# Performance work log

Measured on AMD Instinct MI355X. Metric: run time of the kernel, lower is better.

Reference implementation:

```python
import jax, jax.numpy as jnp
import numpy as np

N_NODES = 8192
D = 384
N_EDGES = 262144
N_REL = 4
N_LAYERS = 2
BATCH = 64


def setup_inputs() -> dict:
    key = jax.random.key(0)
    ks = jax.random.split(key, 8)
    x = jax.random.normal(ks[0], (N_NODES, D), jnp.float32)
    edge_index = jax.random.randint(ks[1], (2, N_EDGES), 0, N_NODES, dtype=jnp.int32)
    edge_type = jax.random.randint(ks[2], (N_EDGES,), 0, N_REL, dtype=jnp.int32)
    s = 1.0 / np.sqrt(D)
    W_rel = jax.random.uniform(ks[3], (N_LAYERS, N_REL, D, D), jnp.float32, -s, s)
    b_rel = jnp.zeros((N_LAYERS, N_REL, D), jnp.float32)
    norm_const = jnp.ones((N_LAYERS, N_REL), jnp.float32)
    W_msg = jax.random.uniform(ks[4], (N_LAYERS, D, D), jnp.float32, -s, s)
    b_msg = jnp.zeros((N_LAYERS, D), jnp.float32)
    W_self = jax.random.uniform(ks[5], (N_LAYERS, D, D), jnp.float32, -s, s)
    b_self = jnp.zeros((N_LAYERS, D), jnp.float32)
    bn_gamma = jnp.ones((D,), jnp.float32)
    bn_beta = jnp.zeros((D,), jnp.float32)
    return {"x": x, "edge_index": edge_index, "edge_type": edge_type,
            "bn_gamma": bn_gamma, "bn_beta": bn_beta,
            "W_rel": W_rel, "b_rel": b_rel, "norm_const": norm_const,
            "W_msg": W_msg, "b_msg": b_msg, "W_self": W_self, "b_self": b_self,
            "batch_size": BATCH}


def _seg_sum(v, idx, n):
    return jax.ops.segment_sum(v, idx, num_segments=n)


def _forward(x, bn_gamma, bn_beta, W_rel, b_rel, norm_const, W_msg, b_msg,
             W_self, b_self, edge_index, edge_type, batch_size):
    n = x.shape[0]
    # BatchNorm1d (training-mode batch stats) on the utterance embeddings
    mu = x.mean(axis=0)
    var = x.var(axis=0)
    h = bn_gamma * (x - mu) * jax.lax.rsqrt(var + 1e-5) + bn_beta
    src, dst = edge_index[0], edge_index[1]  # PyG: row=source(j), col=target(i)
    # pairwise cosine similarity, gathered only at the edges actually used:
    # edge_weights[dst, src] = <h_dst, h_src> / (|h_dst||h_src|)
    xn = h / jnp.linalg.norm(h, axis=1, keepdims=True)
    w_e = jnp.sum(xn[dst] * xn[src], axis=-1)  # [E]
    ones_e = jnp.ones(src.shape[0], jnp.float32)
    n_layers, n_rel = W_rel.shape[0], W_rel.shape[1]
    for l in range(n_layers):
        # RelationAwareMP: per-relation linear + weighted scatter-mean, summed
        out = jnp.zeros((n, W_rel.shape[2]), h.dtype)
        for r in range(n_rel):
            mask = (edge_type == r).astype(h.dtype)  # [E]
            xr = h @ W_rel[l, r].T + b_rel[l, r]  # [N, D]
            coef = mask * w_e / norm_const[l, r]  # [E]
            s = _seg_sum(coef[:, None] * xr[src], dst, n)
            c = _seg_sum(mask, dst, n)
            out = out + s / jnp.maximum(c, 1.0)[:, None]
        rel_out = jax.nn.relu(out)
        # MP: relu(mean_j lin(x_j) + self_lin(x)), then residual
        mj = rel_out @ W_msg[l].T + b_msg[l]
        s = _seg_sum(mj[src], dst, n)
        c = _seg_sum(ones_e, dst, n)
        aggr = s / jnp.maximum(c, 1.0)[:, None]
        h = jax.nn.relu(aggr + rel_out @ W_self[l].T + b_self[l]) + h
    return h.reshape(batch_size, -1, h.shape[-1]).mean(axis=1)


def reference(x, edge_index, edge_type, bn_gamma, bn_beta, W_rel, b_rel,
              norm_const, W_msg, b_msg, W_self, b_self, batch_size):
    return _forward(x, bn_gamma, bn_beta, W_rel, b_rel, norm_const,
                    W_msg, b_msg, W_self, b_self,
                    edge_index, edge_type, batch_size)
```

## Files before the change

kernel.cpp:

```cpp
#include <hip/hip_runtime.h>
#include <hip/hip_bf16.h>

#define NN 8192
#define DD 384
#define NE 262144
#define NR 4
#define NL 2
#define NB 64

typedef __attribute__((ext_vector_type(8))) short bf16x8;
typedef __attribute__((ext_vector_type(4))) float f32x4;

__device__ __forceinline__ unsigned short f2bf(float f) {
  unsigned u = __float_as_uint(f);
  unsigned r = (u + 0x7fffu + ((u >> 16) & 1u)) >> 16;
  return (unsigned short)r;
}
__device__ __forceinline__ unsigned pack_bf2(float lo, float hi) {
  return (unsigned)f2bf(lo) | ((unsigned)f2bf(hi) << 16);
}
__device__ __forceinline__ float bflo(unsigned u) { return __uint_as_float(u << 16); }
__device__ __forceinline__ float bfhi(unsigned u) { return __uint_as_float(u & 0xffff0000u); }
__device__ __forceinline__ void gl_lds16(const void* g, void* l) {
  __builtin_amdgcn_global_load_lds(
      (const __attribute__((address_space(1))) unsigned int*)g,
      (__attribute__((address_space(3))) unsigned int*)l, 16, 0, 0);
}
__device__ __forceinline__ float dot8(uint4 a, uint4 b) {
  return bflo(a.x) * bflo(b.x) + bfhi(a.x) * bfhi(b.x) +
         bflo(a.y) * bflo(b.y) + bfhi(a.y) * bfhi(b.y) +
         bflo(a.z) * bflo(b.z) + bfhi(a.z) * bfhi(b.z) +
         bflo(a.w) * bflo(b.w) + bfhi(a.w) * bfhi(b.w);
}

__global__ void k_zero(uint4* __restrict__ p, int n4) {
  int i = blockIdx.x * 256 + threadIdx.x;
  if (i < n4) p[i] = make_uint4(0, 0, 0, 0);
}

__global__ void k_colstats(const float* __restrict__ x, float* __restrict__ musum,
                           float* __restrict__ msqsum) {
  int c = threadIdx.x;
  int r0 = blockIdx.x * 32;
  float s = 0.f, s2 = 0.f;
  for (int r = 0; r < 32; ++r) {
    float v = x[(size_t)(r0 + r) * DD + c];
    s += v; s2 += v * v;
  }
  atomicAdd(&musum[c], s);
  atomicAdd(&msqsum[c], s2);
}

__global__ void k_bn(const float* __restrict__ x, const float* __restrict__ gamma,
                     const float* __restrict__ beta, const float* __restrict__ musum,
                     const float* __restrict__ msqsum, float* __restrict__ h,
                     short* __restrict__ h_bf, float* __restrict__ ninv) {
  int n = blockIdx.x;
  int t = threadIdx.x;
  float ss = 0.f;
#pragma unroll
  for (int i = 0; i < 6; ++i) {
    int c = t + i * 64;
    float m = musum[c] * (1.f / NN);
    float var = msqsum[c] * (1.f / NN) - m * m;
    float v = gamma[c] * (x[(size_t)n * DD + c] - m) * rsqrtf(var + 1e-5f) + beta[c];
    h[(size_t)n * DD + c] = v;
    h_bf[(size_t)n * DD + c] = (short)f2bf(v);
    ss += v * v;
  }
#pragma unroll
  for (int m = 32; m; m >>= 1) ss += __shfl_xor(ss, m, 64);
  if (t == 0) ninv[n] = rsqrtf(ss);
}

__global__ void k_counts(const int* __restrict__ ei, const int* __restrict__ et,
                         int* __restrict__ c_rel) {
  int e = blockIdx.x * blockDim.x + threadIdx.x;
  if (e >= NE) return;
  int dst = ei[NE + e];
  atomicAdd(&c_rel[dst * NR + et[e]], 1);
}

__global__ void k_scan(const int* __restrict__ c_rel, int* __restrict__ rp2,
                       int* __restrict__ cursor) {
  __shared__ int part[1024];
  int t = threadIdx.x;
  int base = t * 32;
  int v[32]; int s = 0;
#pragma unroll
  for (int i = 0; i < 32; ++i) { v[i] = c_rel[base + i]; s += v[i]; }
  part[t] = s;
  __syncthreads();
  for (int off = 1; off < 1024; off <<= 1) {
    int add = (t >= off) ? part[t - off] : 0;
    __syncthreads();
    part[t] += add;
    __syncthreads();
  }
  int run = (t == 0) ? 0 : part[t - 1];
  if (t == 0) rp2[0] = 0;
#pragma unroll
  for (int i = 0; i < 32; ++i) {
    cursor[base + i] = run;
    run += v[i];
    rp2[base + i + 1] = run;
  }
}

__global__ void k_fill(const int* __restrict__ ei, const int* __restrict__ et,
                       int* __restrict__ cursor, int* __restrict__ meta) {
  int e = blockIdx.x * blockDim.x + threadIdx.x;
  if (e >= NE) return;
  int src = ei[e], dst = ei[NE + e];
  int pos = atomicAdd(&cursor[dst * NR + et[e]], 1);
  meta[pos] = src;
}

__global__ void k_we2(const short* __restrict__ hb, const float* __restrict__ ninv,
                      const int* __restrict__ rp2, const int* __restrict__ meta,
                      float* __restrict__ wsort) {
  int n = blockIdx.x;
  int g = threadIdx.x >> 4, sl = threadIdx.x & 15;
  int beg = rp2[n * 4], end = rp2[n * 4 + 4];
  if (beg == end) return;
  const uint4* hd = (const uint4*)(hb + (size_t)n * DD);
  uint4 b0 = hd[sl], b1 = hd[16 + sl], b2 = hd[32 + sl];
  float nd = ninv[n];
  for (int s = beg + g; s < end; s += 16) {
    int src = meta[s];
    const uint4* hs = (const uint4*)(hb + (size_t)src * DD);
    float acc = dot8(hs[sl], b0) + dot8(hs[16 + sl], b1) + dot8(hs[32 + sl], b2);
#pragma unroll
    for (int m = 8; m; m >>= 1) acc += __shfl_xor(acc, m, 64);
    if (sl == 0) wsort[s] = acc * ninv[src] * nd;
  }
}

__global__ void k_aggrel(const short* __restrict__ hb, const int* __restrict__ rp2,
                         const int* __restrict__ meta, const float* __restrict__ wsort,
                         const float* __restrict__ nc, short* __restrict__ Agg,
                         float* __restrict__ SC, int layer) {
  int n = blockIdx.x;
  int t = threadIdx.x;
  int r = t / 96;
  int i = t - r * 96;
  int beg = rp2[n * 4 + r], end = rp2[n * 4 + r + 1];
  float a0 = 0, a1 = 0, a2 = 0, a3 = 0, s = 0;
  int e = beg;
  for (; e + 3 < end; e += 4) {
    int s0 = meta[e], s1 = meta[e + 1], s2 = meta[e + 2], s3 = meta[e + 3];
    float w0 = wsort[e], w1 = wsort[e + 1], w2 = wsort[e + 2], w3 = wsort[e + 3];
    uint2 u0 = ((const uint2*)(hb + (size_t)s0 * DD))[i];
    uint2 u1 = ((const uint2*)(hb + (size_t)s1 * DD))[i];
    uint2 u2 = ((const uint2*)(hb + (size_t)s2 * DD))[i];
    uint2 u3 = ((const uint2*)(hb + (size_t)s3 * DD))[i];
    a0 += w0 * bflo(u0.x) + w1 * bflo(u1.x) + w2 * bflo(u2.x) + w3 * bflo(u3.x);
    a1 += w0 * bfhi(u0.x) + w1 * bfhi(u1.x) + w2 * bfhi(u2.x) + w3 * bfhi(u3.x);
    a2 += w0 * bflo(u0.y) + w1 * bflo(u1.y) + w2 * bflo(u2.y) + w3 * bflo(u3.y);
    a3 += w0 * bfhi(u0.y) + w1 * bfhi(u1.y) + w2 * bfhi(u2.y) + w3 * bfhi(u3.y);
    s += w0 + w1 + w2 + w3;
  }
  for (; e < end; ++e) {
    int s0 = meta[e];
    float w0 = wsort[e];
    uint2 u0 = ((const uint2*)(hb + (size_t)s0 * DD))[i];
    a0 += w0 * bflo(u0.x); a1 += w0 * bfhi(u0.x);
    a2 += w0 * bflo(u0.y); a3 += w0 * bfhi(u0.y);
    s += w0;
  }
  int c = end - beg;
  float f = 1.f / (nc[layer * 4 + r] * (float)(c > 1 ? c : 1));
  uint2 o;
  o.x = pack_bf2(a0 * f, a1 * f);
  o.y = pack_bf2(a2 * f, a3 * f);
  ((uint2*)(Agg + (size_t)n * 1536 + r * 384))[i] = o;
  if (i == 0) SC[n * 4 + r] = s * f;
}

__global__ void k_aggmp(short* __restrict__ B1, const int* __restrict__ rp2,
                        const int* __restrict__ meta) {
  __shared__ float red[3][96][4];
  int n = blockIdx.x;
  int t = threadIdx.x;
  int g = t / 96, i = t - g * 96;
  int beg = rp2[n * 4], end = rp2[n * 4 + 4];
  float a0 = 0, a1 = 0, a2 = 0, a3 = 0;
  int e = beg + g;
  for (; e + 12 < end; e += 16) {
    int s0 = meta[e], s1 = meta[e + 4], s2 = meta[e + 8], s3 = meta[e + 12];
    uint2 u0 = ((const uint2*)(B1 + (size_t)s0 * 768 + 384))[i];
    uint2 u1 = ((const uint2*)(B1 + (size_t)s1 * 768 + 384))[i];
    uint2 u2 = ((const uint2*)(B1 + (size_t)s2 * 768 + 384))[i];
    uint2 u3 = ((const uint2*)(B1 + (size_t)s3 * 768 + 384))[i];
    a0 += bflo(u0.x) + bflo(u1.x) + bflo(u2.x) + bflo(u3.x);
    a1 += bfhi(u0.x) + bfhi(u1.x) + bfhi(u2.x) + bfhi(u3.x);
    a2 += bflo(u0.y) + bflo(u1.y) + bflo(u2.y) + bflo(u3.y);
    a3 += bfhi(u0.y) + bfhi(u1.y) + bfhi(u2.y) + bfhi(u3.y);
  }
  for (; e < end; e += 4) {
    int s0 = meta[e];
    uint2 u = ((const uint2*)(B1 + (size_t)s0 * 768 + 384))[i];
    a0 += bflo(u.x); a1 += bfhi(u.x);
    a2 += bflo(u.y); a3 += bfhi(u.y);
  }
  if (g) {
    red[g - 1][i][0] = a0; red[g - 1][i][1] = a1;
    red[g - 1][i][2] = a2; red[g - 1][i][3] = a3;
  }
  __syncthreads();
  if (g == 0) {
#pragma unroll
    for (int k = 0; k < 3; ++k) {
      a0 += red[k][i][0]; a1 += red[k][i][1];
      a2 += red[k][i][2]; a3 += red[k][i][3];
    }
    float inv = (end > beg) ? 1.f / (float)(end - beg) : 0.f;
    uint2 o;
    o.x = pack_bf2(a0 * inv, a1 * inv);
    o.y = pack_bf2(a2 * inv, a3 * inv);
    ((uint2*)(B1 + (size_t)n * 768))[i] = o;
  }
}

__global__ void k_packall(const float* __restrict__ W_rel, const float* __restrict__ W_msg,
                          const float* __restrict__ W_self, short* __restrict__ Wcat,
                          short* __restrict__ Wcat2) {
  const int T1 = NL * 384 * 1536;
  const int T2 = NL * 384 * 768;
  int idx = blockIdx.x * blockDim.x + threadIdx.x;
  if (idx < T1) {
    int l = idx / (384 * 1536);
    int rem = idx - l * 384 * 1536;
    int i = rem / 1536, kk = rem - i * 1536;
    int r = kk / 384, k = kk - r * 384;
    Wcat[idx] = (short)f2bf(W_rel[(((size_t)(l * NR + r) * DD) + i) * DD + k]);
  } else if (idx < T1 + T2) {
    int j = idx - T1;
    int l = j / (384 * 768);
    int rem = j - l * 384 * 768;
    int i = rem / 768, kk = rem - i * 768;
    float v = (kk < 384) ? W_msg[((size_t)l * DD + i) * DD + kk]
                         : W_self[((size_t)l * DD + i) * DD + kk - 384];
    Wcat2[j] = (short)f2bf(v);
  }
}

template <int MODE>
__global__ __launch_bounds__(256) void k_gemm_mfma(
    const short* __restrict__ A, int K, const short* __restrict__ Bp,
    const float* __restrict__ SC, const float* __restrict__ brel_l,
    const float* __restrict__ bmsg_l, const float* __restrict__ bself_l,
    const int* __restrict__ rp2, float* __restrict__ h,
    short* __restrict__ h_bf, short* __restrict__ Cout) {
  __shared__ short As[2][64 * 64];
  __shared__ short Bs[2][64 * 64];
  int tid = threadIdx.x;
  int lane = tid & 63;
  int w = tid >> 6;
  int wr = w >> 1, wc = w & 1;
  int bm = blockIdx.x, bn = blockIdx.y;

  int r0 = (w << 3) + (lane >> 3);
  int qg = (lane & 7) ^ (r0 & 7);
  const short* Ag0 = A + (size_t)(bm * 64 + r0) * K + qg * 8;
  const short* Ag1 = A + (size_t)(bm * 64 + r0 + 32) * K + qg * 8;
  const short* Bg0 = Bp + (size_t)(bn * 64 + r0) * K + qg * 8;
  const short* Bg1 = Bp + (size_t)(bn * 64 + r0 + 32) * K + qg * 8;

  auto stage = [&](int bi, int k0) {
    gl_lds16(Ag0 + k0, &As[bi][w * 512]);
    gl_lds16(Ag1 + k0, &As[bi][2048 + w * 512]);
    gl_lds16(Bg0 + k0, &Bs[bi][w * 512]);
    gl_lds16(Bg1 + k0, &Bs[bi][2048 + w * 512]);
  };

  f32x4 acc[2][2] = {};
  int fr = lane & 15, fq = lane >> 4;
  int nt = K >> 6;
  stage(0, 0);
  __syncthreads();
  for (int t = 0; t < nt; ++t) {
    if (t + 1 < nt) stage((t + 1) & 1, (t + 1) << 6);
    const short* Ab = As[t & 1];
    const short* Bb = Bs[t & 1];
#pragma unroll
    for (int kk = 0; kk < 2; ++kk) {
      bf16x8 a[2], b[2];
#pragma unroll
      for (int i = 0; i < 2; ++i) {
        int r = wr * 32 + i * 16 + fr;
        int qs = (kk * 4 + fq) ^ (r & 7);
        a[i] = *(const bf16x8*)&Ab[r * 64 + qs * 8];
      }
#pragma unroll
      for (int j = 0; j < 2; ++j) {
        int r = wc * 32 + j * 16 + fr;
        int qs = (kk * 4 + fq) ^ (r & 7);
        b[j] = *(const bf16x8*)&Bb[r * 64 + qs * 8];
      }
#pragma unroll
      for (int i = 0; i < 2; ++i)
#pragma unroll
        for (int j = 0; j < 2; ++j)
          acc[i][j] = __builtin_amdgcn_mfma_f32_16x16x32_bf16(a[i], b[j], acc[i][j], 0, 0, 0);
    }
    __syncthreads();
  }

  int cr = (lane >> 4) * 4;
  int cc = lane & 15;
#pragma unroll
  for (int i = 0; i < 2; ++i) {
#pragma unroll
    for (int jj = 0; jj < 4; ++jj) {
      int row = bm * 64 + wr * 32 + i * 16 + cr + jj;
      if (MODE == 0) {
        float4 sc = *(const float4*)&SC[row * 4];
#pragma unroll
        for (int j = 0; j < 2; ++j) {
          int col = bn * 64 + wc * 32 + j * 16 + cc;
          float v = acc[i][j][jj] + sc.x * brel_l[col] + sc.y * brel_l[384 + col] +
                    sc.z * brel_l[768 + col] + sc.w * brel_l[1152 + col];
          Cout[(size_t)row * 768 + 384 + col] = (short)f2bf(fmaxf(v, 0.f));
        }
      } else {
        float bmul = (rp2[(row + 1) * 4] > rp2[row * 4]) ? 1.f : 0.f;
#pragma unroll
        for (int j = 0; j < 2; ++j) {
          int col = bn * 64 + wc * 32 + j * 16 + cc;
          float v = acc[i][j][jj] + bmul * bmsg_l[col] + bself_l[col];
          float o = fmaxf(v, 0.f) + h[(size_t)row * DD + col];
          h[(size_t)row * DD + col] = o;
          h_bf[(size_t)row * DD + col] = (short)f2bf(o);
        }
      }
    }
  }
}

__global__ void k_out(const float* __restrict__ h, float* __restrict__ out) {
  int b = blockIdx.x;
  int c = threadIdx.x;
  float s = 0.f;
  for (int j = 0; j < 128; ++j) s += h[(size_t)(b * 128 + j) * DD + c];
  out[b * DD + c] = s * (1.f / 128.f);
}

extern "C" void kernel_launch(void* const* d_in, const int* in_sizes, int n_in,
                              void* d_out, int out_size, void* d_ws, size_t ws_size,
                              hipStream_t stream) {
  const float* x      = (const float*)d_in[0];
  const int*   ei     = (const int*)d_in[1];
  const int*   et     = (const int*)d_in[2];
  const float* gamma  = (const float*)d_in[3];
  const float* beta   = (const float*)d_in[4];
  const float* W_rel  = (const float*)d_in[5];
  const float* b_rel  = (const float*)d_in[6];
  const float* nc     = (const float*)d_in[7];
  const float* W_msg  = (const float*)d_in[8];
  const float* b_msg  = (const float*)d_in[9];
  const float* W_self = (const float*)d_in[10];
  const float* b_self = (const float*)d_in[11];
  float* out = (float*)d_out;

  char* ws = (char*)d_ws;
  size_t off = 0;
  auto alloc = [&](size_t bytes) -> void* {
    void* p = ws + off;
    off = (off + bytes + 255) & ~(size_t)255;
    return p;
  };
  float* h      = (float*)alloc((size_t)NN * DD * 4);
  short* h_bf   = (short*)alloc((size_t)NN * DD * 2);
  short* Agg    = (short*)alloc((size_t)NN * 1536 * 2);
  short* B1     = (short*)alloc((size_t)NN * 768 * 2);
  short* Wcat   = (short*)alloc((size_t)NL * 384 * 1536 * 2);
  short* Wcat2  = (short*)alloc((size_t)NL * 384 * 768 * 2);
  float* SC     = (float*)alloc((size_t)NN * 4 * 4);
  int*   meta   = (int*)alloc((size_t)NE * 4);
  float* wsort  = (float*)alloc((size_t)NE * 4);
  int*   rp2    = (int*)alloc((size_t)(NN * 4 + 1) * 4);
  int*   cursor = (int*)alloc((size_t)NN * 4 * 4);
  float* ninv   = (float*)alloc((size_t)NN * 4);
  char*  zb     = (char*)alloc(134144);
  float* musum  = (float*)(zb);
  float* msqsum = (float*)(zb + 1536);
  int*   c_rel  = (int*)(zb + 3072);

  k_zero<<<(134144 / 16 + 255) / 256, 256, 0, stream>>>((uint4*)zb, 134144 / 16);
  k_colstats<<<256, 384, 0, stream>>>(x, musum, msqsum);
  k_bn<<<NN, 64, 0, stream>>>(x, gamma, beta, musum, msqsum, h, h_bf, ninv);
  k_counts<<<NE / 256, 256, 0, stream>>>(ei, et, c_rel);
  k_scan<<<1, 1024, 0, stream>>>(c_rel, rp2, cursor);
  k_fill<<<NE / 256, 256, 0, stream>>>(ei, et, cursor, meta);
  k_we2<<<NN, 256, 0, stream>>>(h_bf, ninv, rp2, meta, wsort);
  k_packall<<<(NL * 384 * 1536 + NL * 384 * 768 + 255) / 256, 256, 0, stream>>>(
      W_rel, W_msg, W_self, Wcat, Wcat2);

  for (int l = 0; l < NL; ++l) {
    k_aggrel<<<NN, 384, 0, stream>>>(h_bf, rp2, meta, wsort, nc, Agg, SC, l);
    k_gemm_mfma<0><<<dim3(128, 6), 256, 0, stream>>>(
        Agg, 1536, Wcat + (size_t)l * 384 * 1536, SC, b_rel + l * NR * DD,
        nullptr, nullptr, nullptr, nullptr, nullptr, B1);
    k_aggmp<<<NN, 384, 0, stream>>>(B1, rp2, meta);
    k_gemm_mfma<1><<<dim3(128, 6), 256, 0, stream>>>(
        B1, 768, Wcat2 + (size_t)l * 384 * 768, nullptr, nullptr,
        b_msg + l * DD, b_self + l * DD, rp2, h, h_bf, nullptr);
  }
  k_out<<<64, 384, 0, stream>>>(h, out);
}
```

Baseline: 304.3 us.

## Merge preprocessing kernels and deepen gather unrolling in edge aggregation kernels

Column statistics, per-relation edge counting and weight packing are merged into one launch so the independent work shares a single grid and two kernel launches go away. The cosine-weight kernel now gives each edge 8 lanes instead of 16, so more edges are processed per pass with a shorter shuffle reduction. The relation and message aggregation loops issue 8 independent row gathers before accumulating, to keep more memory requests in flight. The cost is higher register pressure and more divergent control flow inside the merged kernel.

```diff
diff --git a/kernel.cpp b/kernel.cpp
--- a/kernel.cpp
+++ b/kernel.cpp
@@ -38,17 +38,49 @@
   if (i < n4) p[i] = make_uint4(0, 0, 0, 0);
 }
 
-__global__ void k_colstats(const float* __restrict__ x, float* __restrict__ musum,
-                           float* __restrict__ msqsum) {
-  int c = threadIdx.x;
-  int r0 = blockIdx.x * 32;
-  float s = 0.f, s2 = 0.f;
-  for (int r = 0; r < 32; ++r) {
-    float v = x[(size_t)(r0 + r) * DD + c];
-    s += v; s2 += v * v;
-  }
-  atomicAdd(&musum[c], s);
-  atomicAdd(&msqsum[c], s2);
+__global__ void k_pre(const float* __restrict__ x, float* __restrict__ musum,
+                      float* __restrict__ msqsum, const int* __restrict__ ei,
+                      const int* __restrict__ et, int* __restrict__ c_rel,
+                      const float* __restrict__ W_rel, const float* __restrict__ W_msg,
+                      const float* __restrict__ W_self, short* __restrict__ Wcat,
+                      short* __restrict__ Wcat2) {
+  int b = blockIdx.x;
+  int t = threadIdx.x;
+  if (b < 256) {
+    int c = t;
+    int r0 = b * 32;
+    float s = 0.f, s2 = 0.f;
+    for (int r = 0; r < 32; ++r) {
+      float v = x[(size_t)(r0 + r) * DD + c];
+      s += v; s2 += v * v;
+    }
+    atomicAdd(&musum[c], s);
+    atomicAdd(&msqsum[c], s2);
+  } else if (b < 939) {
+    int e = (b - 256) * 384 + t;
+    if (e < NE) {
+      int dst = ei[NE + e];
+      atomicAdd(&c_rel[dst * NR + et[e]], 1);
+    }
+  } else {
+    const int T1 = NL * 384 * 1536;
+    int idx = (b - 939) * 384 + t;
+    if (idx < T1) {
+      int l = idx / (384 * 1536);
+      int rem = idx - l * 384 * 1536;
+      int i = rem / 1536, kk = rem - i * 1536;
+      int r = kk / 384, k = kk - r * 384;
+      Wcat[idx] = (short)f2bf(W_rel[(((size_t)(l * NR + r) * DD) + i) * DD + k]);
+    } else {
+      int j = idx - T1;
+      int l = j / (384 * 768);
+      int rem = j - l * 384 * 768;
+      int i = rem / 768, kk = rem - i * 768;
+      float v = (kk < 384) ? W_msg[((size_t)l * DD + i) * DD + kk]
+                           : W_self[((size_t)l * DD + i) * DD + kk - 384];
+      Wcat2[j] = (short)f2bf(v);
+    }
+  }
 }
 
 __global__ void k_bn(const float* __restrict__ x, const float* __restrict__ gamma,
@@ -73,14 +105,6 @@
   if (t == 0) ninv[n] = rsqrtf(ss);
 }
 
-__global__ void k_counts(const int* __restrict__ ei, const int* __restrict__ et,
-                         int* __restrict__ c_rel) {
-  int e = blockIdx.x * blockDim.x + threadIdx.x;
-  if (e >= NE) return;
-  int dst = ei[NE + e];
-  atomicAdd(&c_rel[dst * NR + et[e]], 1);
-}
-
 __global__ void k_scan(const int* __restrict__ c_rel, int* __restrict__ rp2,
                        int* __restrict__ cursor) {
   __shared__ int part[1024];
@@ -120,18 +144,20 @@
                       const int* __restrict__ rp2, const int* __restrict__ meta,
                       float* __restrict__ wsort) {
   int n = blockIdx.x;
-  int g = threadIdx.x >> 4, sl = threadIdx.x & 15;
+  int g = threadIdx.x >> 3, sl = threadIdx.x & 7;
   int beg = rp2[n * 4], end = rp2[n * 4 + 4];
   if (beg == end) return;
   const uint4* hd = (const uint4*)(hb + (size_t)n * DD);
-  uint4 b0 = hd[sl], b1 = hd[16 + sl], b2 = hd[32 + sl];
+  uint4 b0 = hd[sl], b1 = hd[8 + sl], b2 = hd[16 + sl];
+  uint4 b3 = hd[24 + sl], b4 = hd[32 + sl], b5 = hd[40 + sl];
   float nd = ninv[n];
-  for (int s = beg + g; s < end; s += 16) {
+  for (int s = beg + g; s < end; s += 32) {
     int src = meta[s];
     const uint4* hs = (const uint4*)(hb + (size_t)src * DD);
-    float acc = dot8(hs[sl], b0) + dot8(hs[16 + sl], b1) + dot8(hs[32 + sl], b2);
-#pragma unroll
-    for (int m = 8; m; m >>= 1) acc += __shfl_xor(acc, m, 64);
+    float acc = dot8(hs[sl], b0) + dot8(hs[8 + sl], b1) + dot8(hs[16 + sl], b2) +
+                dot8(hs[24 + sl], b3) + dot8(hs[32 + sl], b4) + dot8(hs[40 + sl], b5);
+#pragma unroll
+    for (int m = 4; m; m >>= 1) acc += __shfl_xor(acc, m, 64);
     if (sl == 0) wsort[s] = acc * ninv[src] * nd;
   }
 }
@@ -147,18 +173,36 @@
   int beg = rp2[n * 4 + r], end = rp2[n * 4 + r + 1];
   float a0 = 0, a1 = 0, a2 = 0, a3 = 0, s = 0;
   int e = beg;
-  for (; e + 3 < end; e += 4) {
-    int s0 = meta[e], s1 = meta[e + 1], s2 = meta[e + 2], s3 = meta[e + 3];
-    float w0 = wsort[e], w1 = wsort[e + 1], w2 = wsort[e + 2], w3 = wsort[e + 3];
-    uint2 u0 = ((const uint2*)(hb + (size_t)s0 * DD))[i];
-    uint2 u1 = ((const uint2*)(hb + (size_t)s1 * DD))[i];
-    uint2 u2 = ((const uint2*)(hb + (size_t)s2 * DD))[i];
-    uint2 u3 = ((const uint2*)(hb + (size_t)s3 * DD))[i];
-    a0 += w0 * bflo(u0.x) + w1 * bflo(u1.x) + w2 * bflo(u2.x) + w3 * bflo(u3.x);
-    a1 += w0 * bfhi(u0.x) + w1 * bfhi(u1.x) + w2 * bfhi(u2.x) + w3 * bfhi(u3.x);
-    a2 += w0 * bflo(u0.y) + w1 * bflo(u1.y) + w2 * bflo(u2.y) + w3 * bflo(u3.y);
-    a3 += w0 * bfhi(u0.y) + w1 * bfhi(u1.y) + w2 * bfhi(u2.y) + w3 * bfhi(u3.y);
-    s += w0 + w1 + w2 + w3;
+  for (; e + 7 < end; e += 8) {
+    uint2 u[8]; float wv[8];
+#pragma unroll
+    for (int q = 0; q < 8; ++q) {
+      int sq = meta[e + q];
+      wv[q] = wsort[e + q];
+      u[q] = ((const uint2*)(hb + (size_t)sq * DD))[i];
+    }
+#pragma unroll
+    for (int q = 0; q < 8; ++q) {
+      a0 += wv[q] * bflo(u[q].x); a1 += wv[q] * bfhi(u[q].x);
+      a2 += wv[q] * bflo(u[q].y); a3 += wv[q] * bfhi(u[q].y);
+      s += wv[q];
+    }
+  }
+  if (e + 3 < end) {
+    uint2 u[4]; float wv[4];
+#pragma unroll
+    for (int q = 0; q < 4; ++q) {
+      int sq = meta[e + q];
+      wv[q] = wsort[e + q];
+      u[q] = ((const uint2*)(hb + (size_t)sq * DD))[i];
+    }
+#pragma unroll
+    for (int q = 0; q < 4; ++q) {
+      a0 += wv[q] * bflo(u[q].x); a1 += wv[q] * bfhi(u[q].x);
+      a2 += wv[q] * bflo(u[q].y); a3 += wv[q] * bfhi(u[q].y);
+      s += wv[q];
+    }
+    e += 4;
   }
   for (; e < end; ++e) {
     int s0 = meta[e];
@@ -186,16 +230,18 @@
   int beg = rp2[n * 4], end = rp2[n * 4 + 4];
   float a0 = 0, a1 = 0, a2 = 0, a3 = 0;
   int e = beg + g;
-  for (; e + 12 < end; e += 16) {
-    int s0 = meta[e], s1 = meta[e + 4], s2 = meta[e + 8], s3 = meta[e + 12];
-    uint2 u0 = ((const uint2*)(B1 + (size_t)s0 * 768 + 384))[i];
-    uint2 u1 = ((const uint2*)(B1 + (size_t)s1 * 768 + 384))[i];
-    uint2 u2 = ((const uint2*)(B1 + (size_t)s2 * 768 + 384))[i];
-    uint2 u3 = ((const uint2*)(B1 + (size_t)s3 * 768 + 384))[i];
-    a0 += bflo(u0.x) + bflo(u1.x) + bflo(u2.x) + bflo(u3.x);
-    a1 += bfhi(u0.x) + bfhi(u1.x) + bfhi(u2.x) + bfhi(u3.x);
-    a2 += bflo(u0.y) + bflo(u1.y) + bflo(u2.y) + bflo(u3.y);
-    a3 += bfhi(u0.y) + bfhi(u1.y) + bfhi(u2.y) + bfhi(u3.y);
+  for (; e + 28 < end; e += 32) {
+    uint2 u[8];
+#pragma unroll
+    for (int q = 0; q < 8; ++q) {
+      int sq = meta[e + q * 4];
+      u[q] = ((const uint2*)(B1 + (size_t)sq * 768 + 384))[i];
+    }
+#pragma unroll
+    for (int q = 0; q < 8; ++q) {
+      a0 += bflo(u[q].x); a1 += bfhi(u[q].x);
+      a2 += bflo(u[q].y); a3 += bfhi(u[q].y);
+    }
   }
   for (; e < end; e += 4) {
     int s0 = meta[e];
@@ -219,29 +265,6 @@
     o.x = pack_bf2(a0 * inv, a1 * inv);
     o.y = pack_bf2(a2 * inv, a3 * inv);
     ((uint2*)(B1 + (size_t)n * 768))[i] = o;
-  }
-}
-
-__global__ void k_packall(const float* __restrict__ W_rel, const float* __restrict__ W_msg,
-                          const float* __restrict__ W_self, short* __restrict__ Wcat,
-                          short* __restrict__ Wcat2) {
-  const int T1 = NL * 384 * 1536;
-  const int T2 = NL * 384 * 768;
-  int idx = blockIdx.x * blockDim.x + threadIdx.x;
-  if (idx < T1) {
-    int l = idx / (384 * 1536);
-    int rem = idx - l * 384 * 1536;
-    int i = rem / 1536, kk = rem - i * 1536;
-    int r = kk / 384, k = kk - r * 384;
-    Wcat[idx] = (short)f2bf(W_rel[(((size_t)(l * NR + r) * DD) + i) * DD + k]);
-  } else if (idx < T1 + T2) {
-    int j = idx - T1;
-    int l = j / (384 * 768);
-    int rem = j - l * 384 * 768;
-    int i = rem / 768, kk = rem - i * 768;
-    float v = (kk < 384) ? W_msg[((size_t)l * DD + i) * DD + kk]
-                         : W_self[((size_t)l * DD + i) * DD + kk - 384];
-    Wcat2[j] = (short)f2bf(v);
   }
 }
 
@@ -388,14 +411,12 @@
   int*   c_rel  = (int*)(zb + 3072);
 
   k_zero<<<(134144 / 16 + 255) / 256, 256, 0, stream>>>((uint4*)zb, 134144 / 16);
-  k_colstats<<<256, 384, 0, stream>>>(x, musum, msqsum);
+  k_pre<<<5547, 384, 0, stream>>>(x, musum, msqsum, ei, et, c_rel,
+                                  W_rel, W_msg, W_self, Wcat, Wcat2);
   k_bn<<<NN, 64, 0, stream>>>(x, gamma, beta, musum, msqsum, h, h_bf, ninv);
-  k_counts<<<NE / 256, 256, 0, stream>>>(ei, et, c_rel);
   k_scan<<<1, 1024, 0, stream>>>(c_rel, rp2, cursor);
   k_fill<<<NE / 256, 256, 0, stream>>>(ei, et, cursor, meta);
   k_we2<<<NN, 256, 0, stream>>>(h_bf, ninv, rp2, meta, wsort);
-  k_packall<<<(NL * 384 * 1536 + NL * 384 * 768 + 255) / 256, 256, 0, stream>>>(
-      W_rel, W_msg, W_self, Wcat, Wcat2);
 
   for (int l = 0; l < NL; ++l) {
     k_aggrel<<<NN, 384, 0, stream>>>(h_bf, rp2, meta, wsort, nc, Agg, SC, l);
```

New measurement: 313.5 us. 3.0% more time.
